# Kernel optimization log

Hardware: AMD Instinct MI355X
Metric: run time of the kernel (lower is better)

The kernel has to match this reference:

```python
import jax, jax.numpy as jnp
import numpy as np

B, T, C, H = 2, 2048, 1024, 16
D = C // H            # head dim = 64
MAXREL = 32           # max_relative_position


def setup_inputs() -> dict:
    key = jax.random.key(0)
    ks = jax.random.split(key, 4)
    s = lambda n: 1.0 / np.sqrt(n).astype(np.float32)
    return {
        "x": jax.random.normal(ks[0], (B, T, C), jnp.float32),
        # causal mask, as produced by torch.tril buffer `bias`
        "mask": jnp.tril(jnp.ones((1, 1, T, T), jnp.float32)),
        "w_attn": jax.random.normal(ks[1], (C, 3 * C), jnp.float32) * s(C),
        "b_attn": jnp.zeros((3 * C,), jnp.float32),
        "w_proj": jax.random.normal(ks[2], (C, C), jnp.float32) * s(C),
        "b_proj": jnp.zeros((C,), jnp.float32),
        "rel_k_table": jax.random.normal(ks[3], (2 * MAXREL + 1, D), jnp.float32) * s(D),
    }


def reference(x, mask, w_attn, b_attn, w_proj, b_proj, rel_k_table):
    # qkv projection and head split
    qkv = x @ w_attn + b_attn                              # [B,T,3C]
    q, k, v = jnp.split(qkv, 3, axis=-1)
    to_heads = lambda t: t.reshape(B, T, H, D).transpose(0, 2, 1, 3)  # [B,H,T,D]
    q, k, v = to_heads(q), to_heads(k), to_heads(v)

    # content-content scores
    attn1 = jnp.einsum('bhqd,bhkd->bhqk', q, k)            # [B,H,T,T]

    # content-position scores via relative-position embedding gather
    dist = jnp.arange(T)[None, :] - jnp.arange(T)[:, None]
    idx = jnp.clip(dist, -MAXREL, MAXREL) + MAXREL         # [T,T] in [0, 2*MAXREL]
    rel_k = rel_k_table[idx]                               # [T,T,D]
    attn2 = jnp.einsum('bhqd,qkd->bhqk', q, rel_k)         # [B,H,T,T]

    att = (attn1 + attn2) * (1.0 / np.sqrt(D).astype(np.float32))
    att = jnp.where(mask[:, :, :T, :T] == 0, -jnp.inf, att)
    att = jax.nn.softmax(att, axis=-1)
    att = jnp.nan_to_num(att, nan=0.0)                     # fully-masked rows -> 0
    post_soft_att = att                                    # dropout is identity (eval)

    y = jnp.einsum('bhqk,bhkd->bhqd', att, v)              # [B,H,T,D]
    y = y.transpose(0, 2, 1, 3).reshape(B, T, C)
    y = y @ w_proj + b_proj
    return y, post_soft_att
```

## Files before the change

kernel.cpp:

```cpp
#include <hip/hip_runtime.h>


typedef __bf16 bf16x8 __attribute__((ext_vector_type(8)));
typedef float f32x4 __attribute__((ext_vector_type(4)));
typedef unsigned short u16x8 __attribute__((ext_vector_type(8)));

__device__ __forceinline__ unsigned short f2bf(float f) {
  unsigned u = __float_as_uint(f);
  u += 0x7fff + ((u >> 16) & 1);
  return (unsigned short)(u >> 16);
}
__device__ __forceinline__ float bf2f(unsigned short s) {
  return __uint_as_float(((unsigned)s) << 16);
}

__global__ __launch_bounds__(256)
void cvt_split(const float* __restrict__ in, unsigned short* __restrict__ hi,
               unsigned short* __restrict__ lo, int n4) {
  int i = blockIdx.x * 256 + threadIdx.x;
  if (i >= n4) return;
  float4 v = ((const float4*)in)[i];
  ushort4 h, l;
  h.x = f2bf(v.x); l.x = f2bf(v.x - bf2f(h.x));
  h.y = f2bf(v.y); l.y = f2bf(v.y - bf2f(h.y));
  h.z = f2bf(v.z); l.z = f2bf(v.z - bf2f(h.z));
  h.w = f2bf(v.w); l.w = f2bf(v.w - bf2f(h.w));
  ((ushort4*)hi)[i] = h;
  ((ushort4*)lo)[i] = l;
}

__global__ __launch_bounds__(256)
void cvt_split_T(const float* __restrict__ in, unsigned short* __restrict__ hiT,
                 unsigned short* __restrict__ loT, int K, int N) {
  __shared__ float tile[64][65];
  const int tid = threadIdx.x;
  const int bc = blockIdx.x * 64;
  const int br = blockIdx.y * 64;
#pragma unroll
  for (int j = 0; j < 4; ++j) {
    int f = tid + j * 256;
    int r = f >> 4, c4 = (f & 15) << 2;
    *(float4*)&tile[r][c4] = *(const float4*)&in[(size_t)(br + r) * N + bc + c4];
  }
  __syncthreads();
#pragma unroll
  for (int j = 0; j < 4; ++j) {
    int f = tid + j * 256;
    int n = f >> 4, k4 = (f & 15) << 2;
    ushort4 h, l;
    float v;
    v = tile[k4 + 0][n]; h.x = f2bf(v); l.x = f2bf(v - bf2f(h.x));
    v = tile[k4 + 1][n]; h.y = f2bf(v); l.y = f2bf(v - bf2f(h.y));
    v = tile[k4 + 2][n]; h.z = f2bf(v); l.z = f2bf(v - bf2f(h.z));
    v = tile[k4 + 3][n]; h.w = f2bf(v); l.w = f2bf(v - bf2f(h.w));
    size_t o = (size_t)(bc + n) * K + br + k4;
    *(ushort4*)&hiT[o] = h;
    *(ushort4*)&loT[o] = l;
  }
}

__device__ __forceinline__ int swz(int row, int k) {
  return row * 32 + ((((k >> 3) ^ row) & 3) << 3) + (k & 7);
}

__global__ __launch_bounds__(256)
void mfma_gemm_bias(const unsigned short* __restrict__ Ah,
                    const unsigned short* __restrict__ Al,
                    const unsigned short* __restrict__ Bth,
                    const unsigned short* __restrict__ Btl,
                    const float* __restrict__ bias, float* __restrict__ C,
                    int M, int N, int K) {
  __shared__ unsigned short As_h[128 * 32], As_l[128 * 32];
  __shared__ unsigned short Bs_h[128 * 32], Bs_l[128 * 32];
  const int tid = threadIdx.x;
  const int bm = blockIdx.y * 128, bn = blockIdx.x * 128;
  const int l = tid & 63, w = tid >> 6;
  const int wm = (w >> 1) * 64, wn = (w & 1) * 64;
  const int fr = l & 15, kg = (l >> 4) << 3;

  const int u0 = tid, u1 = tid + 256;
  const int m0s = u0 >> 2, k0s = (u0 & 3) << 3;
  const int m1s = u1 >> 2, k1s = (u1 & 3) << 3;

  f32x4 acc[4][4];
#pragma unroll
  for (int i = 0; i < 4; ++i)
#pragma unroll
    for (int j = 0; j < 4; ++j) {
      acc[i][j].x = 0.f; acc[i][j].y = 0.f; acc[i][j].z = 0.f; acc[i][j].w = 0.f;
    }

  u16x8 rah0, rah1, ral0, ral1, rbh0, rbh1, rbl0, rbl1;
  {
    const size_t a0 = (size_t)(bm + m0s) * K + k0s, a1 = (size_t)(bm + m1s) * K + k1s;
    const size_t b0 = (size_t)(bn + m0s) * K + k0s, b1 = (size_t)(bn + m1s) * K + k1s;
    rah0 = *(const u16x8*)&Ah[a0];  rah1 = *(const u16x8*)&Ah[a1];
    ral0 = *(const u16x8*)&Al[a0];  ral1 = *(const u16x8*)&Al[a1];
    rbh0 = *(const u16x8*)&Bth[b0]; rbh1 = *(const u16x8*)&Bth[b1];
    rbl0 = *(const u16x8*)&Btl[b0]; rbl1 = *(const u16x8*)&Btl[b1];
  }

  const int nk = K >> 5;
  for (int ks = 0; ks < nk; ++ks) {
    __syncthreads();
    *(u16x8*)&As_h[swz(m0s, k0s)] = rah0;  *(u16x8*)&As_h[swz(m1s, k1s)] = rah1;
    *(u16x8*)&As_l[swz(m0s, k0s)] = ral0;  *(u16x8*)&As_l[swz(m1s, k1s)] = ral1;
    *(u16x8*)&Bs_h[swz(m0s, k0s)] = rbh0;  *(u16x8*)&Bs_h[swz(m1s, k1s)] = rbh1;
    *(u16x8*)&Bs_l[swz(m0s, k0s)] = rbl0;  *(u16x8*)&Bs_l[swz(m1s, k1s)] = rbl1;
    __syncthreads();
    if (ks + 1 < nk) {
      const int k0 = (ks + 1) << 5;
      const size_t a0 = (size_t)(bm + m0s) * K + k0 + k0s,
                   a1 = (size_t)(bm + m1s) * K + k0 + k1s;
      const size_t b0 = (size_t)(bn + m0s) * K + k0 + k0s,
                   b1 = (size_t)(bn + m1s) * K + k0 + k1s;
      rah0 = *(const u16x8*)&Ah[a0];  rah1 = *(const u16x8*)&Ah[a1];
      ral0 = *(const u16x8*)&Al[a0];  ral1 = *(const u16x8*)&Al[a1];
      rbh0 = *(const u16x8*)&Bth[b0]; rbh1 = *(const u16x8*)&Bth[b1];
      rbl0 = *(const u16x8*)&Btl[b0]; rbl1 = *(const u16x8*)&Btl[b1];
    }
    bf16x8 ah[4], al[4], bh[4], bl[4];
#pragma unroll
    for (int i = 0; i < 4; ++i) {
      ah[i] = *(bf16x8*)&As_h[swz(wm + i * 16 + fr, kg)];
      al[i] = *(bf16x8*)&As_l[swz(wm + i * 16 + fr, kg)];
      bh[i] = *(bf16x8*)&Bs_h[swz(wn + i * 16 + fr, kg)];
      bl[i] = *(bf16x8*)&Bs_l[swz(wn + i * 16 + fr, kg)];
    }
#pragma unroll
    for (int mi = 0; mi < 4; ++mi)
#pragma unroll
      for (int ni = 0; ni < 4; ++ni) {
        acc[mi][ni] = __builtin_amdgcn_mfma_f32_16x16x32_bf16(
            ah[mi], bh[ni], acc[mi][ni], 0, 0, 0);
        acc[mi][ni] = __builtin_amdgcn_mfma_f32_16x16x32_bf16(
            ah[mi], bl[ni], acc[mi][ni], 0, 0, 0);
        acc[mi][ni] = __builtin_amdgcn_mfma_f32_16x16x32_bf16(
            al[mi], bh[ni], acc[mi][ni], 0, 0, 0);
      }
  }

#pragma unroll
  for (int mi = 0; mi < 4; ++mi) {
    const int rowb = bm + wm + mi * 16 + (l >> 4) * 4;
#pragma unroll
    for (int ni = 0; ni < 4; ++ni) {
      const int col = bn + wn + ni * 16 + fr;
      const float bv = bias[col];
      C[(size_t)(rowb + 0) * N + col] = acc[mi][ni].x + bv;
      C[(size_t)(rowb + 1) * N + col] = acc[mi][ni].y + bv;
      C[(size_t)(rowb + 2) * N + col] = acc[mi][ni].z + bv;
      C[(size_t)(rowb + 3) * N + col] = acc[mi][ni].w + bv;
    }
  }
}

__global__ __launch_bounds__(256)
void relproj_kernel(const float* __restrict__ qkv, const float* __restrict__ tbl_g,
                    float* __restrict__ proj) {
  __shared__ float tbl[65 * 65];
  __shared__ float qsh[4 * 64];
  const int tid = threadIdx.x;
  for (int i = tid; i < 65 * 64; i += 256) {
    int r = i >> 6, d = i & 63;
    tbl[r * 65 + d] = tbl_g[i];
  }
  const int w = tid >> 6, lane = tid & 63;
  const int rid = blockIdx.x * 4 + w;
  const int b = rid >> 15, h = (rid >> 11) & 15, q = rid & 2047;
  qsh[w * 64 + lane] =
      qkv[(size_t)(b * 2048 + q) * 3072 + h * 64 + lane];
  __syncthreads();
  float acc = 0.f;
#pragma unroll
  for (int d = 0; d < 64; ++d)
    acc = fmaf(qsh[w * 64 + d], tbl[lane * 65 + d], acc);
  proj[(size_t)rid * 65 + lane] = acc;
  float part = qsh[w * 64 + lane] * tbl[64 * 65 + lane];
#pragma unroll
  for (int off = 32; off; off >>= 1) part += __shfl_xor(part, off, 64);
  if (lane == 0) proj[(size_t)rid * 65 + 64] = part;
}

__global__ __launch_bounds__(512)
void attn_kernel(const float* __restrict__ qkv, const float* __restrict__ proj,
                 float* __restrict__ att, float* __restrict__ ymid) {
  __shared__ float p_s[16 * 2048];
  __shared__ float kv_s[64 * 68];
  __shared__ float qt[16 * 64];
  __shared__ float pj[16 * 65];
  const int tid = threadIdx.x;
  const int w = tid >> 6, lane = tid & 63;
  const int bh = blockIdx.y;
  const int b = bh >> 4, h = bh & 15;
  const int q0 = blockIdx.x << 4;
  const size_t row_base = (size_t)(b * 2048) * 3072 + h * 64;

  if (tid < 256) {
    int r = tid >> 4, c4 = (tid & 15) << 2;
    *(float4*)&qt[r * 64 + c4] =
        *(const float4*)&qkv[row_base + (size_t)(q0 + r) * 3072 + c4];
  }
  {
    const float* psrc = &proj[((size_t)bh * 2048 + q0) * 65];
    for (int i = tid; i < 16 * 65; i += 512) pj[i] = psrc[i];
  }
  __syncthreads();

  const int r0 = w * 2, r1 = r0 + 1;
  const int qg0 = q0 + r0, qg1 = q0 + r1;
  const int nkt = q0 / 64 + 1;

  float4 q0v[16], q1v[16];
#pragma unroll
  for (int c = 0; c < 16; ++c) {
    q0v[c] = *(float4*)&qt[r0 * 64 + 4 * c];
    q1v[c] = *(float4*)&qt[r1 * 64 + 4 * c];
  }

  float dacc0 = 0.f, dacc1 = 0.f;
  const float* kbase = qkv + row_base + 1024;
  for (int t = 0; t < nkt; ++t) {
    __syncthreads();
#pragma unroll
    for (int j = 0; j < 2; ++j) {
      int f4 = tid + j * 512;
      int kk = f4 >> 4, d4 = (f4 & 15) << 2;
      *(float4*)&kv_s[kk * 68 + d4] =
          *(const float4*)&kbase[(size_t)(t * 64 + kk) * 3072 + d4];
    }
    __syncthreads();
    float a0a = 0.f, a0b = 0.f, a1a = 0.f, a1b = 0.f;
#pragma unroll
    for (int c = 0; c < 16; ++c) {
      float4 kv = *(float4*)&kv_s[lane * 68 + 4 * c];
      a0a = fmaf(q0v[c].x, kv.x, a0a);
      a0b = fmaf(q0v[c].y, kv.y, a0b);
      a0a = fmaf(q0v[c].z, kv.z, a0a);
      a0b = fmaf(q0v[c].w, kv.w, a0b);
      a1a = fmaf(q1v[c].x, kv.x, a1a);
      a1b = fmaf(q1v[c].y, kv.y, a1b);
      a1a = fmaf(q1v[c].z, kv.z, a1a);
      a1b = fmaf(q1v[c].w, kv.w, a1b);
    }
    float acc0 = a0a + a0b, acc1 = a1a + a1b;
    int kg = t * 64 + lane;
    float p0 = 0.f, p1 = 0.f;
    if (kg <= qg0) {
      int dist = qg0 - kg;
      int idx = 32 - (dist > 32 ? 32 : dist);
      p0 = __expf((acc0 + pj[r0 * 65 + idx]) * 0.125f);
      dacc0 += p0;
    }
    if (kg <= qg1) {
      int dist = qg1 - kg;
      int idx = 32 - (dist > 32 ? 32 : dist);
      p1 = __expf((acc1 + pj[r1 * 65 + idx]) * 0.125f);
      dacc1 += p1;
    }
    p_s[r0 * 2048 + kg] = p0;
    p_s[r1 * 2048 + kg] = p1;
  }

#pragma unroll
  for (int off = 32; off; off >>= 1) {
    dacc0 += __shfl_xor(dacc0, off, 64);
    dacc1 += __shfl_xor(dacc1, off, 64);
  }
  const float inv0 = 1.f / dacc0, inv1 = 1.f / dacc1;

  float* att0 = &att[((size_t)bh * 2048 + qg0) * 2048];
  float* att1 = &att[((size_t)bh * 2048 + qg1) * 2048];

  for (int t = nkt; t < 32; ++t) {
    att0[t * 64 + lane] = 0.f;
    att1[t * 64 + lane] = 0.f;
  }

  const float* vbase = qkv + row_base + 2048;
  float y0a = 0.f, y0b = 0.f, y1a = 0.f, y1b = 0.f;
  for (int t = 0; t < nkt; ++t) {
    __syncthreads();
#pragma unroll
    for (int j = 0; j < 2; ++j) {
      int idx = tid + j * 512;
      int d = idx & 63, k4 = idx >> 6;
      const float* src = &vbase[(size_t)(t * 64 + 4 * k4) * 3072 + d];
      float4 vv;
      vv.x = src[0];
      vv.y = src[3072];
      vv.z = src[6144];
      vv.w = src[9216];
      *(float4*)&kv_s[d * 64 + 4 * (k4 ^ (d & 15))] = vv;
    }
    __syncthreads();
#pragma unroll
    for (int c = 0; c < 16; ++c) {
      float4 vv = *(float4*)&kv_s[lane * 64 + 4 * (c ^ (lane & 15))];
      float4 pb0 = *(float4*)&p_s[r0 * 2048 + t * 64 + 4 * c];
      float4 pb1 = *(float4*)&p_s[r1 * 2048 + t * 64 + 4 * c];
      y0a = fmaf(pb0.x, vv.x, y0a);
      y0b = fmaf(pb0.y, vv.y, y0b);
      y0a = fmaf(pb0.z, vv.z, y0a);
      y0b = fmaf(pb0.w, vv.w, y0b);
      y1a = fmaf(pb1.x, vv.x, y1a);
      y1b = fmaf(pb1.y, vv.y, y1b);
      y1a = fmaf(pb1.z, vv.z, y1a);
      y1b = fmaf(pb1.w, vv.w, y1b);
    }
    att0[t * 64 + lane] = p_s[r0 * 2048 + t * 64 + lane] * inv0;
    att1[t * 64 + lane] = p_s[r1 * 2048 + t * 64 + lane] * inv1;
  }
  ymid[(size_t)(b * 2048 + qg0) * 1024 + h * 64 + lane] = (y0a + y0b) * inv0;
  ymid[(size_t)(b * 2048 + qg1) * 1024 + h * 64 + lane] = (y1a + y1b) * inv1;
}

extern "C" void kernel_launch(void* const* d_in, const int* in_sizes, int n_in,
                              void* d_out, int out_size, void* d_ws, size_t ws_size,
                              hipStream_t stream) {
  const float* x       = (const float*)d_in[0];
  const float* w_attn  = (const float*)d_in[2];
  const float* b_attn  = (const float*)d_in[3];
  const float* w_proj  = (const float*)d_in[4];
  const float* b_proj  = (const float*)d_in[5];
  const float* rel_tbl = (const float*)d_in[6];

  float* out = (float*)d_out;
  float* att = out + (size_t)2 * 2048 * 1024;

  float* qkv  = (float*)d_ws;
  float* proj = qkv + (size_t)12582912;
  float* ymid = proj + (size_t)4259840;
  unsigned short* xh  = (unsigned short*)(ymid + (size_t)4194304);
  unsigned short* xl  = xh + (size_t)4194304;
  unsigned short* wah = xl + (size_t)4194304;
  unsigned short* wal = wah + (size_t)3145728;
  unsigned short* wph = wal + (size_t)3145728;
  unsigned short* wpl = wph + (size_t)1048576;

  cvt_split<<<4096, 256, 0, stream>>>(x, xh, xl, 1048576);
  cvt_split_T<<<dim3(48, 16), 256, 0, stream>>>(w_attn, wah, wal, 1024, 3072);
  cvt_split_T<<<dim3(16, 16), 256, 0, stream>>>(w_proj, wph, wpl, 1024, 1024);

  mfma_gemm_bias<<<dim3(24, 32), 256, 0, stream>>>(xh, xl, wah, wal, b_attn,
                                                   qkv, 4096, 3072, 1024);
  relproj_kernel<<<16384, 256, 0, stream>>>(qkv, rel_tbl, proj);
  attn_kernel<<<dim3(128, 32), 512, 0, stream>>>(qkv, proj, att, ymid);
  cvt_split<<<4096, 256, 0, stream>>>(ymid, xh, xl, 1048576);
  mfma_gemm_bias<<<dim3(8, 32), 256, 0, stream>>>(xh, xl, wph, wpl, b_proj,
                                                  out, 4096, 1024, 1024);
}
```

Before: 1.485 ms.

## Fuse QK and PV passes with double-buffered K/V tiles and separate normalization

The attention kernel now computes unnormalized probabilities and accumulates P·V in a single pass over key tiles. It double-buffers K and V in shared memory with register prefetch, which removes the 128KB per-row probability buffer and the second K/V pass. Unnormalized probabilities are written straight to the output, and a new att_norm kernel rescales them by the stored inverse denominators and zero-fills the masked region. The trade-off is an extra read-modify-write over the full 512MB attention matrix in exchange for higher occupancy and fewer global loads and barriers. It also drops the max-subtraction in the softmax exactly as before, and it reuses the w_attn workspace for the inverse denominators after the QKV GEMM.

```diff
diff --git a/kernel.cpp b/kernel.cpp
--- a/kernel.cpp
+++ b/kernel.cpp
@@ -182,11 +182,13 @@
   if (lane == 0) proj[(size_t)rid * 65 + 64] = part;
 }
 
-__global__ __launch_bounds__(512)
-void attn_kernel(const float* __restrict__ qkv, const float* __restrict__ proj,
-                 float* __restrict__ att, float* __restrict__ ymid) {
-  __shared__ float p_s[16 * 2048];
-  __shared__ float kv_s[64 * 68];
+__global__ __launch_bounds__(512, 4)
+void attn_fused(const float* __restrict__ qkv, const float* __restrict__ proj,
+                float* __restrict__ att, float* __restrict__ ymid,
+                float* __restrict__ dinv) {
+  __shared__ float kv_k[2][64 * 68];
+  __shared__ float kv_v[2][64 * 64];
+  __shared__ float p_s[16 * 68];
   __shared__ float qt[16 * 64];
   __shared__ float pj[16 * 65];
   const int tid = threadIdx.x;
@@ -205,46 +207,70 @@
     const float* psrc = &proj[((size_t)bh * 2048 + q0) * 65];
     for (int i = tid; i < 16 * 65; i += 512) pj[i] = psrc[i];
   }
-  __syncthreads();
 
   const int r0 = w * 2, r1 = r0 + 1;
   const int qg0 = q0 + r0, qg1 = q0 + r1;
   const int nkt = q0 / 64 + 1;
 
-  float4 q0v[16], q1v[16];
-#pragma unroll
-  for (int c = 0; c < 16; ++c) {
-    q0v[c] = *(float4*)&qt[r0 * 64 + 4 * c];
-    q1v[c] = *(float4*)&qt[r1 * 64 + 4 * c];
-  }
+  const float* kbase = qkv + row_base + 1024;
+  const float* vbase = qkv + row_base + 2048;
+
+  const int kk0 = tid >> 4, d40 = (tid & 15) << 2;
+  const int kk1 = kk0 + 32;
+  const int dA = tid & 63, k4A = tid >> 6;
+  const int k4B = k4A + 8;
+
+  float4 rk0, rk1, rv0, rv1;
+
+#define LOAD_TILE(t)                                                        \
+  {                                                                         \
+    rk0 = *(const float4*)&kbase[(size_t)((t) * 64 + kk0) * 3072 + d40];    \
+    rk1 = *(const float4*)&kbase[(size_t)((t) * 64 + kk1) * 3072 + d40];    \
+    const float* s0 = &vbase[(size_t)((t) * 64 + 4 * k4A) * 3072 + dA];     \
+    rv0.x = s0[0]; rv0.y = s0[3072]; rv0.z = s0[6144]; rv0.w = s0[9216];    \
+    const float* s1 = &vbase[(size_t)((t) * 64 + 4 * k4B) * 3072 + dA];     \
+    rv1.x = s1[0]; rv1.y = s1[3072]; rv1.z = s1[6144]; rv1.w = s1[9216];    \
+  }
+#define STORE_TILE(bi)                                                      \
+  {                                                                         \
+    *(float4*)&kv_k[bi][kk0 * 68 + d40] = rk0;                              \
+    *(float4*)&kv_k[bi][kk1 * 68 + d40] = rk1;                              \
+    *(float4*)&kv_v[bi][dA * 64 + 4 * (k4A ^ (dA & 15))] = rv0;             \
+    *(float4*)&kv_v[bi][dA * 64 + 4 * (k4B ^ (dA & 15))] = rv1;             \
+  }
+
+  LOAD_TILE(0);
+  STORE_TILE(0);
+  if (nkt > 1) LOAD_TILE(1);
+  __syncthreads();
 
   float dacc0 = 0.f, dacc1 = 0.f;
-  const float* kbase = qkv + row_base + 1024;
+  float y0a = 0.f, y0b = 0.f, y1a = 0.f, y1b = 0.f;
+  float* att0 = &att[((size_t)bh * 2048 + qg0) * 2048];
+  float* att1 = &att[((size_t)bh * 2048 + qg1) * 2048];
+
   for (int t = 0; t < nkt; ++t) {
-    __syncthreads();
-#pragma unroll
-    for (int j = 0; j < 2; ++j) {
-      int f4 = tid + j * 512;
-      int kk = f4 >> 4, d4 = (f4 & 15) << 2;
-      *(float4*)&kv_s[kk * 68 + d4] =
-          *(const float4*)&kbase[(size_t)(t * 64 + kk) * 3072 + d4];
-    }
-    __syncthreads();
+    const int cur = t & 1;
+    if (t + 1 < nkt) STORE_TILE(cur ^ 1);
+    if (t + 2 < nkt) LOAD_TILE(t + 2);
+
     float a0a = 0.f, a0b = 0.f, a1a = 0.f, a1b = 0.f;
 #pragma unroll
     for (int c = 0; c < 16; ++c) {
-      float4 kv = *(float4*)&kv_s[lane * 68 + 4 * c];
-      a0a = fmaf(q0v[c].x, kv.x, a0a);
-      a0b = fmaf(q0v[c].y, kv.y, a0b);
-      a0a = fmaf(q0v[c].z, kv.z, a0a);
-      a0b = fmaf(q0v[c].w, kv.w, a0b);
-      a1a = fmaf(q1v[c].x, kv.x, a1a);
-      a1b = fmaf(q1v[c].y, kv.y, a1b);
-      a1a = fmaf(q1v[c].z, kv.z, a1a);
-      a1b = fmaf(q1v[c].w, kv.w, a1b);
+      float4 kv = *(float4*)&kv_k[cur][lane * 68 + 4 * c];
+      float4 qa = *(float4*)&qt[r0 * 64 + 4 * c];
+      float4 qb = *(float4*)&qt[r1 * 64 + 4 * c];
+      a0a = fmaf(qa.x, kv.x, a0a);
+      a0b = fmaf(qa.y, kv.y, a0b);
+      a0a = fmaf(qa.z, kv.z, a0a);
+      a0b = fmaf(qa.w, kv.w, a0b);
+      a1a = fmaf(qb.x, kv.x, a1a);
+      a1b = fmaf(qb.y, kv.y, a1b);
+      a1a = fmaf(qb.z, kv.z, a1a);
+      a1b = fmaf(qb.w, kv.w, a1b);
     }
     float acc0 = a0a + a0b, acc1 = a1a + a1b;
-    int kg = t * 64 + lane;
+    const int kg = t * 64 + lane;
     float p0 = 0.f, p1 = 0.f;
     if (kg <= qg0) {
       int dist = qg0 - kg;
@@ -258,47 +284,16 @@
       p1 = __expf((acc1 + pj[r1 * 65 + idx]) * 0.125f);
       dacc1 += p1;
     }
-    p_s[r0 * 2048 + kg] = p0;
-    p_s[r1 * 2048 + kg] = p1;
-  }
-
-#pragma unroll
-  for (int off = 32; off; off >>= 1) {
-    dacc0 += __shfl_xor(dacc0, off, 64);
-    dacc1 += __shfl_xor(dacc1, off, 64);
-  }
-  const float inv0 = 1.f / dacc0, inv1 = 1.f / dacc1;
-
-  float* att0 = &att[((size_t)bh * 2048 + qg0) * 2048];
-  float* att1 = &att[((size_t)bh * 2048 + qg1) * 2048];
-
-  for (int t = nkt; t < 32; ++t) {
-    att0[t * 64 + lane] = 0.f;
-    att1[t * 64 + lane] = 0.f;
-  }
-
-  const float* vbase = qkv + row_base + 2048;
-  float y0a = 0.f, y0b = 0.f, y1a = 0.f, y1b = 0.f;
-  for (int t = 0; t < nkt; ++t) {
-    __syncthreads();
-#pragma unroll
-    for (int j = 0; j < 2; ++j) {
-      int idx = tid + j * 512;
-      int d = idx & 63, k4 = idx >> 6;
-      const float* src = &vbase[(size_t)(t * 64 + 4 * k4) * 3072 + d];
-      float4 vv;
-      vv.x = src[0];
-      vv.y = src[3072];
-      vv.z = src[6144];
-      vv.w = src[9216];
-      *(float4*)&kv_s[d * 64 + 4 * (k4 ^ (d & 15))] = vv;
-    }
-    __syncthreads();
+    p_s[r0 * 68 + lane] = p0;
+    p_s[r1 * 68 + lane] = p1;
+    att0[t * 64 + lane] = p0;
+    att1[t * 64 + lane] = p1;
+
 #pragma unroll
     for (int c = 0; c < 16; ++c) {
-      float4 vv = *(float4*)&kv_s[lane * 64 + 4 * (c ^ (lane & 15))];
-      float4 pb0 = *(float4*)&p_s[r0 * 2048 + t * 64 + 4 * c];
-      float4 pb1 = *(float4*)&p_s[r1 * 2048 + t * 64 + 4 * c];
+      float4 vv = *(float4*)&kv_v[cur][lane * 64 + 4 * (c ^ (lane & 15))];
+      float4 pb0 = *(float4*)&p_s[r0 * 68 + 4 * c];
+      float4 pb1 = *(float4*)&p_s[r1 * 68 + 4 * c];
       y0a = fmaf(pb0.x, vv.x, y0a);
       y0b = fmaf(pb0.y, vv.y, y0b);
       y0a = fmaf(pb0.z, vv.z, y0a);
@@ -308,11 +303,56 @@
       y1a = fmaf(pb1.z, vv.z, y1a);
       y1b = fmaf(pb1.w, vv.w, y1b);
     }
-    att0[t * 64 + lane] = p_s[r0 * 2048 + t * 64 + lane] * inv0;
-    att1[t * 64 + lane] = p_s[r1 * 2048 + t * 64 + lane] * inv1;
+    __syncthreads();
+  }
+#undef LOAD_TILE
+#undef STORE_TILE
+
+#pragma unroll
+  for (int off = 32; off; off >>= 1) {
+    dacc0 += __shfl_xor(dacc0, off, 64);
+    dacc1 += __shfl_xor(dacc1, off, 64);
+  }
+  const float inv0 = 1.f / dacc0, inv1 = 1.f / dacc1;
+  if (lane == 0) {
+    dinv[(size_t)bh * 2048 + qg0] = inv0;
+    dinv[(size_t)bh * 2048 + qg1] = inv1;
   }
   ymid[(size_t)(b * 2048 + qg0) * 1024 + h * 64 + lane] = (y0a + y0b) * inv0;
   ymid[(size_t)(b * 2048 + qg1) * 1024 + h * 64 + lane] = (y1a + y1b) * inv1;
+}
+
+__global__ __launch_bounds__(256)
+void att_norm(float* __restrict__ att, const float* __restrict__ dinv) {
+  const size_t row = blockIdx.x;
+  const int q = (int)(row & 2047);
+  const float inv = dinv[row];
+  float* p = att + row * 2048;
+  const int c0 = threadIdx.x * 8;
+  if (c0 + 7 <= q) {
+    float4 a = *(float4*)&p[c0];
+    float4 c = *(float4*)&p[c0 + 4];
+    a.x *= inv; a.y *= inv; a.z *= inv; a.w *= inv;
+    c.x *= inv; c.y *= inv; c.z *= inv; c.w *= inv;
+    *(float4*)&p[c0] = a;
+    *(float4*)&p[c0 + 4] = c;
+  } else if (c0 > q) {
+    float4 z = {0.f, 0.f, 0.f, 0.f};
+    *(float4*)&p[c0] = z;
+    *(float4*)&p[c0 + 4] = z;
+  } else {
+    float4 a, c;
+    a.x = (c0 + 0 <= q) ? p[c0 + 0] * inv : 0.f;
+    a.y = (c0 + 1 <= q) ? p[c0 + 1] * inv : 0.f;
+    a.z = (c0 + 2 <= q) ? p[c0 + 2] * inv : 0.f;
+    a.w = (c0 + 3 <= q) ? p[c0 + 3] * inv : 0.f;
+    c.x = (c0 + 4 <= q) ? p[c0 + 4] * inv : 0.f;
+    c.y = (c0 + 5 <= q) ? p[c0 + 5] * inv : 0.f;
+    c.z = (c0 + 6 <= q) ? p[c0 + 6] * inv : 0.f;
+    c.w = (c0 + 7 <= q) ? p[c0 + 7] * inv : 0.f;
+    *(float4*)&p[c0] = a;
+    *(float4*)&p[c0 + 4] = c;
+  }
 }
 
 extern "C" void kernel_launch(void* const* d_in, const int* in_sizes, int n_in,
@@ -337,6 +377,7 @@
   unsigned short* wal = wah + (size_t)3145728;
   unsigned short* wph = wal + (size_t)3145728;
   unsigned short* wpl = wph + (size_t)1048576;
+  float* dinv = (float*)wah;
 
   cvt_split<<<4096, 256, 0, stream>>>(x, xh, xl, 1048576);
   cvt_split_T<<<dim3(48, 16), 256, 0, stream>>>(w_attn, wah, wal, 1024, 3072);
@@ -345,7 +386,8 @@
   mfma_gemm_bias<<<dim3(24, 32), 256, 0, stream>>>(xh, xl, wah, wal, b_attn,
                                                    qkv, 4096, 3072, 1024);
   relproj_kernel<<<16384, 256, 0, stream>>>(qkv, rel_tbl, proj);
-  attn_kernel<<<dim3(128, 32), 512, 0, stream>>>(qkv, proj, att, ymid);
+  attn_fused<<<dim3(128, 32), 512, 0, stream>>>(qkv, proj, att, ymid, dinv);
+  att_norm<<<65536, 256, 0, stream>>>(att, dinv);
   cvt_split<<<4096, 256, 0, stream>>>(ymid, xh, xl, 1048576);
   mfma_gemm_bias<<<dim3(8, 32), 256, 0, stream>>>(xh, xl, wph, wpl, b_proj,
                                                   out, 4096, 1024, 1024);
```

Result: slower. 4.154 ms (+179.6%).
